# Kernel tuning notes

Measured on AMD Instinct MI355X. Metric: run time of the kernel, lower is better.

The kernel has to match this reference:

```python
import jax, jax.numpy as jnp
import numpy as np

DIM = 1024          # BIGNET_DIM
LORA = 32
GROUP = 128
N_LIN = 18          # 6 blocks * 3 QLoRALinear
N_LN = 5
EPS = 1e-5


def setup_inputs() -> dict:
    key = jax.random.key(0)
    ks = jax.random.split(key, 8)
    tokens = 16384
    x = jax.random.normal(ks[0], (tokens, DIM), dtype=jnp.float32)
    # int4 codes in [0,16), per-(out,group) scale (block-abs-max norm)
    q = jax.random.randint(ks[1], (N_LIN, DIM, DIM), 0, 16, dtype=jnp.int32)
    norm = jax.random.uniform(ks[2], (N_LIN, DIM, DIM // GROUP), dtype=jnp.float32) * 0.1 + 0.01
    bias = jax.random.normal(ks[3], (N_LIN, DIM), dtype=jnp.float32) * 0.01
    # lora_a: kaiming-uniform * 0.01; lora_b: zeros in the original init, but we use
    # small random values so the LoRA path (and its gradients) are exercised.
    lora_a = jax.random.normal(ks[4], (N_LIN, LORA, DIM), dtype=jnp.float32) * 0.01
    lora_b = jax.random.normal(ks[5], (N_LIN, DIM, LORA), dtype=jnp.float32) * 0.01
    ln_gamma = jnp.ones((N_LN, DIM), dtype=jnp.float32)
    ln_beta = jnp.zeros((N_LN, DIM), dtype=jnp.float32)
    return {"x": x, "q": q, "norm": norm, "bias": bias,
            "lora_a": lora_a, "lora_b": lora_b,
            "ln_gamma": ln_gamma, "ln_beta": ln_beta}


def _dequant(qi, ni):
    # qi: [O, I] int codes in [0,16); ni: [O, I//GROUP] group scales
    O, I = qi.shape
    w = (qi.astype(jnp.float32) / 15.0 * 2.0 - 1.0).reshape(O, I // GROUP, GROUP)
    return (w * ni[..., None]).reshape(O, I)


def _qlora_linear(h, qi, ni, b, la, lb):
    w = _dequant(qi, ni)                      # [O, I]
    base = h @ w.T + b                        # frozen quantized path
    lora = (h @ la.T) @ lb.T                  # rank-32 adapter
    return base + lora


def _layernorm(h, g, b):
    mu = jnp.mean(h, axis=-1, keepdims=True)
    var = jnp.var(h, axis=-1, keepdims=True)
    return (h - mu) * jax.lax.rsqrt(var + EPS) * g + b


def _forward(x, q, norm, bias, lora_a, lora_b, ln_gamma, ln_beta):
    h = x
    for blk in range(6):
        r = h
        for j in range(3):
            i = 3 * blk + j
            r = _qlora_linear(r, q[i], norm[i], bias[i], lora_a[i], lora_b[i])
            if j < 2:
                r = jax.nn.relu(r)
        h = r + h                              # residual
        if blk < 5:
            h = _layernorm(h, ln_gamma[blk], ln_beta[blk])
    return h


def reference(x, q, norm, bias, lora_a, lora_b, ln_gamma, ln_beta):
    return _forward(x, q, norm, bias, lora_a, lora_b, ln_gamma, ln_beta)
```

## Files before the change

### kernel.cpp

```cpp
#include <hip/hip_runtime.h>
#include <stdint.h>


#define TOK   16384
#define DIM   1024
#define NLIN  18
#define EPS   1e-5f

typedef _Float16 f16;
typedef _Float16 f16x8 __attribute__((ext_vector_type(8)));
typedef _Float16 f16x4 __attribute__((ext_vector_type(4)));
typedef float    f32x4 __attribute__((ext_vector_type(4)));

__device__ __forceinline__ void load_lds16(const void* g, void* l) {
  __builtin_amdgcn_global_load_lds(
      (const __attribute__((address_space(1))) void*)g,
      (__attribute__((address_space(3))) void*)l,
      16, 0, 0);
}

__global__ __launch_bounds__(256) void prep_w2(
    const int* __restrict__ q, const float* __restrict__ norm,
    const float* __restrict__ la, const float* __restrict__ lb,
    f16* __restrict__ W)
{
  __shared__ float lbs[128 * 32];
  const int bid   = blockIdx.x;
  const int i     = bid >> 5;
  const int ot    = (bid >> 2) & 7;
  const int ktile = bid & 3;
  const int o0 = ot * 128, k0 = ktile * 256;
  const int tid = threadIdx.x;
  const int kg = tid & 63, og = tid >> 6;
  const int k4 = k0 + kg * 4;

  const float* lbsrc = lb + (size_t)i * DIM * 32 + (size_t)o0 * 32;
  #pragma unroll
  for (int p = 0; p < 4; ++p)
    *(float4*)(lbs + p * 1024 + tid * 4) = *(const float4*)(lbsrc + p * 1024 + tid * 4);

  float4 lar[32];
  const float* lasrc = la + (size_t)i * 32 * DIM + k4;
  #pragma unroll
  for (int r = 0; r < 32; ++r) lar[r] = *(const float4*)(lasrc + r * DIM);
  __syncthreads();

  const float s = 2.f / 15.f;
  for (int oi = 0; oi < 32; ++oi) {
    const int o = o0 + og * 32 + oi;
    const size_t wb = ((size_t)i * DIM + o) * DIM;
    const int4 qv = *(const int4*)(q + wb + k4);
    const float nrm = norm[((size_t)i * DIM + o) * 8 + (k4 >> 7)];
    const float* lbr = lbs + (og * 32 + oi) * 32;
    float ax = 0.f, ay = 0.f, az = 0.f, aw = 0.f;
    #pragma unroll
    for (int r = 0; r < 32; ++r) {
      const float b = lbr[r];
      ax += b * lar[r].x; ay += b * lar[r].y; az += b * lar[r].z; aw += b * lar[r].w;
    }
    f16x4 hv;
    hv[0] = (f16)(((float)qv.x * s - 1.f) * nrm + ax);
    hv[1] = (f16)(((float)qv.y * s - 1.f) * nrm + ay);
    hv[2] = (f16)(((float)qv.z * s - 1.f) * nrm + az);
    hv[3] = (f16)(((float)qv.w * s - 1.f) * nrm + aw);
    *(f16x4*)(W + wb + k4) = hv;
  }
}

__global__ __launch_bounds__(256) void cvt_x(
    const float* __restrict__ x, f16* __restrict__ o)
{
  const size_t idx = ((size_t)blockIdx.x * 256 + threadIdx.x) * 4;
  const float4 v = *(const float4*)(x + idx);
  f16x4 h;
  h[0] = (f16)v.x; h[1] = (f16)v.y; h[2] = (f16)v.z; h[3] = (f16)v.w;
  *(f16x4*)(o + idx) = h;
}

#define BARX()   __builtin_amdgcn_s_barrier()
#define LGKM0()  do { asm volatile("s_waitcnt lgkmcnt(0)" ::: "memory"); \
                      __builtin_amdgcn_sched_barrier(0); } while (0)
#define VMC0()   do { asm volatile("s_waitcnt vmcnt(0)" ::: "memory"); \
                      __builtin_amdgcn_sched_barrier(0); } while (0)

#define RD_AF(so, kk) do { \
  _Pragma("unroll") \
  for (int mi = 0; mi < 8; ++mi) \
    af[mi] = *(const f16x8*)(smem + (so) + arowb[mi] + (ckA ^ ((kk) << 6))); \
} while (0)

#define RD_BF(so, ni0, kk) do { \
  bf[ni0]     = *(const f16x8*)(smem + 65536 + (so) + browb[ni0]     + (ckA ^ ((kk) << 6))); \
  bf[(ni0)+1] = *(const f16x8*)(smem + 65536 + (so) + browb[(ni0)+1] + (ckA ^ ((kk) << 6))); \
} while (0)

#define QUAD(ni0) do { \
  __builtin_amdgcn_s_setprio(1); \
  _Pragma("unroll") \
  for (int mi = 0; mi < 8; ++mi) { \
    acc[mi][ni0]     = __builtin_amdgcn_mfma_f32_16x16x32_f16(af[mi], bf[ni0],     acc[mi][ni0],     0, 0, 0); \
    acc[mi][(ni0)+1] = __builtin_amdgcn_mfma_f32_16x16x32_f16(af[mi], bf[(ni0)+1], acc[mi][(ni0)+1], 0, 0, 0); \
  } \
  __builtin_amdgcn_s_setprio(0); \
} while (0)

#define STAGE_A(kt, dstso) do { \
  _Pragma("unroll") \
  for (int qq = 0; qq < 4; ++qq) \
    load_lds16(gA + (size_t)(kt) * 64 + (size_t)qq * 64 * DIM, \
               smem + (dstso) + qq * 8192 + sdst); \
} while (0)
#define STAGE_B(kt, dstso) do { \
  _Pragma("unroll") \
  for (int qq = 0; qq < 4; ++qq) \
    load_lds16(gB + (size_t)(kt) * 64 + (size_t)qq * 64 * DIM, \
               smem + 65536 + (dstso) + qq * 8192 + sdst); \
} while (0)

template<int EPI>
__global__ __launch_bounds__(512, 2) void gemm3(
    const f16* __restrict__ A, const f16* __restrict__ W,
    const float* __restrict__ bias, const f16* __restrict__ resid,
    void* __restrict__ outp)
{
  __shared__ __align__(16) char smem[131072];

  const int orig = blockIdx.x;
  const int swzb = (orig & 7) * 32 + (orig >> 3);
  const int mt = swzb >> 2, nt = swzb & 3;
  const int t0 = mt * 256, n0 = nt * 256;

  const int tid  = threadIdx.x;
  const int lane = tid & 63;
  const int wid  = tid >> 6;
  const int wm = wid >> 2, wn = wid & 3;

  const int srow = tid >> 3;
  const int sch  = (tid & 7) ^ (srow & 7);
  const f16* gA = A + (size_t)(t0 + srow) * DIM + sch * 8;
  const f16* gB = W + (size_t)(n0 + srow) * DIM + sch * 8;
  const int sdst = tid * 16;

  const int ckA = (((lane >> 4) ^ (lane & 7)) << 4);
  int arowb[8], browb[4];
  #pragma unroll
  for (int mi = 0; mi < 8; ++mi)
    arowb[mi] = (wm * 128 + mi * 16 + (lane & 15)) * 128;
  #pragma unroll
  for (int ni = 0; ni < 4; ++ni)
    browb[ni] = (wn * 64 + ni * 16 + (lane & 15)) * 128;

  f32x4 acc[8][4] = {};
  f16x8 af[8], bf[4];

  STAGE_A(0, 0);
  STAGE_B(0, 0);
  VMC0();
  BARX();

  for (int t = 0; t < 16; ++t) {
    const int so = (t & 1) << 15;
    const int od = ((t + 1) & 1) << 15;
    const bool st = (t < 15);
    RD_AF(so, 0); RD_BF(so, 0, 0);
    if (st) STAGE_A(t + 1, od);
    BARX(); LGKM0(); QUAD(0); BARX();
    RD_BF(so, 2, 0);
    if (st) STAGE_B(t + 1, od);
    BARX(); LGKM0(); QUAD(2); BARX();
    RD_AF(so, 1); RD_BF(so, 0, 1);
    BARX(); LGKM0(); QUAD(0); BARX();
    RD_BF(so, 2, 1);
    VMC0();
    BARX(); LGKM0(); QUAD(2); BARX();
  }

  const int colb = lane & 15;
  const int rowb = (lane >> 4) << 2;
  #pragma unroll
  for (int ni = 0; ni < 4; ++ni) {
    const int col = n0 + wn * 64 + ni * 16 + colb;
    const float bv = bias[col];
    #pragma unroll
    for (int mi = 0; mi < 8; ++mi) {
      const int trow = t0 + wm * 128 + mi * 16 + rowb;
      const f32x4 v = acc[mi][ni];
      #pragma unroll
      for (int r = 0; r < 4; ++r) {
        const size_t idx = (size_t)(trow + r) * DIM + col;
        float val = v[r] + bv;
        if constexpr (EPI == 0) {
          val = fmaxf(val, 0.f);
          ((f16*)outp)[idx] = (f16)val;
        } else if constexpr (EPI == 1) {
          val += (float)resid[idx];
          ((f16*)outp)[idx] = (f16)val;
        } else {
          val += (float)resid[idx];
          ((float*)outp)[idx] = val;
        }
      }
    }
  }
}

__global__ __launch_bounds__(256) void ln_k(
    const f16* __restrict__ in, f16* __restrict__ out,
    const float* __restrict__ g, const float* __restrict__ b)
{
  __shared__ float red[8];
  const int row = blockIdx.x;
  const int tid = threadIdx.x;
  const int c = tid * 4;
  const f16x4 v4 = *(const f16x4*)(in + (size_t)row * DIM + c);
  const float v0 = v4[0], v1 = v4[1], v2 = v4[2], v3 = v4[3];
  float s  = v0 + v1 + v2 + v3;
  float s2 = v0 * v0 + v1 * v1 + v2 * v2 + v3 * v3;
  #pragma unroll
  for (int off = 32; off; off >>= 1) {
    s  += __shfl_xor(s,  off);
    s2 += __shfl_xor(s2, off);
  }
  if ((tid & 63) == 0) { red[(tid >> 6) * 2] = s; red[(tid >> 6) * 2 + 1] = s2; }
  __syncthreads();
  s  = red[0] + red[2] + red[4] + red[6];
  s2 = red[1] + red[3] + red[5] + red[7];
  const float mu  = s * (1.f / DIM);
  const float var = fmaxf(s2 * (1.f / DIM) - mu * mu, 0.f);
  const float rs  = rsqrtf(var + EPS);
  const float4 gv = *(const float4*)(g + c);
  const float4 bv = *(const float4*)(b + c);
  f16x4 o4;
  o4[0] = (f16)((v0 - mu) * rs * gv.x + bv.x);
  o4[1] = (f16)((v1 - mu) * rs * gv.y + bv.y);
  o4[2] = (f16)((v2 - mu) * rs * gv.z + bv.z);
  o4[3] = (f16)((v3 - mu) * rs * gv.w + bv.w);
  *(f16x4*)(out + (size_t)row * DIM + c) = o4;
}

extern "C" void kernel_launch(void* const* d_in, const int* in_sizes, int n_in,
                              void* d_out, int out_size, void* d_ws, size_t ws_size,
                              hipStream_t stream)
{
  (void)in_sizes; (void)n_in; (void)out_size; (void)ws_size;
  const float* x     = (const float*)d_in[0];
  const int*   q     = (const int*)d_in[1];
  const float* norm  = (const float*)d_in[2];
  const float* bias  = (const float*)d_in[3];
  const float* la    = (const float*)d_in[4];
  const float* lb    = (const float*)d_in[5];
  const float* lg    = (const float*)d_in[6];
  const float* lbeta = (const float*)d_in[7];

  char* ws = (char*)d_ws;
  f16* W    = (f16*)ws;
  f16* buf1 = (f16*)(ws + (size_t)NLIN * DIM * DIM * 2);
  f16* buf2 = buf1 + (size_t)TOK * DIM;
  f16* buf0 = (f16*)d_out;
  f16* bufs[3] = {buf0, buf1, buf2};

  prep_w2<<<NLIN * 32, 256, 0, stream>>>(q, norm, la, lb, W);
  cvt_x<<<TOK * DIM / 1024, 256, 0, stream>>>(x, buf0);

  int h = 0;
  for (int blk = 0; blk < 6; ++blk) {
    const int a = (h == 0) ? 1 : 0;
    const int p = 3 - h - a;
    const int i0 = blk * 3;
    const size_t wsz = (size_t)DIM * DIM;
    gemm3<0><<<256, 512, 0, stream>>>(bufs[h], W + (i0 + 0) * wsz,
                                      bias + (i0 + 0) * DIM, nullptr, bufs[a]);
    gemm3<0><<<256, 512, 0, stream>>>(bufs[a], W + (i0 + 1) * wsz,
                                      bias + (i0 + 1) * DIM, nullptr, bufs[p]);
    if (blk < 5) {
      gemm3<1><<<256, 512, 0, stream>>>(bufs[p], W + (i0 + 2) * wsz,
                                        bias + (i0 + 2) * DIM, bufs[h], bufs[a]);
      ln_k<<<TOK, 256, 0, stream>>>(bufs[a], bufs[a], lg + blk * DIM, lbeta + blk * DIM);
      h = a;
    } else {
      gemm3<2><<<256, 512, 0, stream>>>(bufs[p], W + (i0 + 2) * wsz,
                                        bias + (i0 + 2) * DIM, bufs[h], d_out);
    }
  }
}
```

Measured before the change: 1.036 ms.

## Restructure GEMM main loop into a register-double-buffered, deeper-prefetch pipeline

Rewrites the GEMM k-loop so LDS fragment reads for the next MFMA quad are issued before the current quad runs, using separate register sets (afX/afY, several B fragment pairs). A-tiles are now prefetched two k-steps ahead and B-tiles one step ahead, with partial vmcnt waits in place of full drains. The LDS layout moves to per-slot A/B halves, and the explicit lgkmcnt waits are removed. The aim is to hide LDS and global latency behind MFMA work, at the cost of more register pressure and a more delicate hazard ordering.

```diff
diff --git a/kernel.cpp b/kernel.cpp
--- a/kernel.cpp
+++ b/kernel.cpp
@@ -77,48 +77,44 @@
   *(f16x4*)(o + idx) = h;
 }
 
-#define BARX()   __builtin_amdgcn_s_barrier()
-#define LGKM0()  do { asm volatile("s_waitcnt lgkmcnt(0)" ::: "memory"); \
-                      __builtin_amdgcn_sched_barrier(0); } while (0)
-#define VMC0()   do { asm volatile("s_waitcnt vmcnt(0)" ::: "memory"); \
-                      __builtin_amdgcn_sched_barrier(0); } while (0)
-
-#define RD_AF(so, kk) do { \
+#define BARX() __builtin_amdgcn_s_barrier()
+
+#define RD_AF(afd, sl, kk) do { \
   _Pragma("unroll") \
   for (int mi = 0; mi < 8; ++mi) \
-    af[mi] = *(const f16x8*)(smem + (so) + arowb[mi] + (ckA ^ ((kk) << 6))); \
-} while (0)
-
-#define RD_BF(so, ni0, kk) do { \
-  bf[ni0]     = *(const f16x8*)(smem + 65536 + (so) + browb[ni0]     + (ckA ^ ((kk) << 6))); \
-  bf[(ni0)+1] = *(const f16x8*)(smem + 65536 + (so) + browb[(ni0)+1] + (ckA ^ ((kk) << 6))); \
-} while (0)
-
-#define QUAD(ni0) do { \
+    afd[mi] = *(const f16x8*)(smem + (sl) + wmbase + arowb[mi] + (ckA ^ ((kk) << 6))); \
+} while (0)
+
+#define RD_BF(b0, b1, sl, np, kk) do { \
+  b0 = *(const f16x8*)(smem + (sl) + 32768 + wnhalf + browb[(np)*2]     + (ckA ^ ((kk) << 6))); \
+  b1 = *(const f16x8*)(smem + (sl) + 32768 + wnhalf + browb[(np)*2 + 1] + (ckA ^ ((kk) << 6))); \
+} while (0)
+
+#define QUAD(afr, b0, b1, nn) do { \
   __builtin_amdgcn_s_setprio(1); \
   _Pragma("unroll") \
   for (int mi = 0; mi < 8; ++mi) { \
-    acc[mi][ni0]     = __builtin_amdgcn_mfma_f32_16x16x32_f16(af[mi], bf[ni0],     acc[mi][ni0],     0, 0, 0); \
-    acc[mi][(ni0)+1] = __builtin_amdgcn_mfma_f32_16x16x32_f16(af[mi], bf[(ni0)+1], acc[mi][(ni0)+1], 0, 0, 0); \
+    acc[mi][nn]     = __builtin_amdgcn_mfma_f32_16x16x32_f16(afr[mi], b0, acc[mi][nn],     0, 0, 0); \
+    acc[mi][(nn)+1] = __builtin_amdgcn_mfma_f32_16x16x32_f16(afr[mi], b1, acc[mi][(nn)+1], 0, 0, 0); \
   } \
   __builtin_amdgcn_s_setprio(0); \
 } while (0)
 
-#define STAGE_A(kt, dstso) do { \
-  _Pragma("unroll") \
-  for (int qq = 0; qq < 4; ++qq) \
-    load_lds16(gA + (size_t)(kt) * 64 + (size_t)qq * 64 * DIM, \
-               smem + (dstso) + qq * 8192 + sdst); \
-} while (0)
-#define STAGE_B(kt, dstso) do { \
-  _Pragma("unroll") \
-  for (int qq = 0; qq < 4; ++qq) \
-    load_lds16(gB + (size_t)(kt) * 64 + (size_t)qq * 64 * DIM, \
-               smem + 65536 + (dstso) + qq * 8192 + sdst); \
+#define STAGE_A(T, h, dslot) do { \
+  load_lds16(gA + (size_t)((T) * 64) + (size_t)((h) * 128) * DIM, \
+             smem + (dslot) + (h) * 16384 + sdst); \
+  load_lds16(gA + (size_t)((T) * 64) + (size_t)((h) * 128 + 64) * DIM, \
+             smem + (dslot) + (h) * 16384 + 8192 + sdst); \
+} while (0)
+#define STAGE_B(T, h, dslot) do { \
+  load_lds16(gB + (size_t)((T) * 64) + (size_t)((h) * 128) * DIM, \
+             smem + (dslot) + 32768 + (h) * 16384 + sdst); \
+  load_lds16(gB + (size_t)((T) * 64) + (size_t)((h) * 128 + 64) * DIM, \
+             smem + (dslot) + 32768 + (h) * 16384 + 8192 + sdst); \
 } while (0)
 
 template<int EPI>
-__global__ __launch_bounds__(512, 2) void gemm3(
+__global__ __launch_bounds__(512, 2) void gemm4(
     const f16* __restrict__ A, const f16* __restrict__ W,
     const float* __restrict__ bias, const f16* __restrict__ resid,
     void* __restrict__ outp)
@@ -141,38 +137,57 @@
   const f16* gB = W + (size_t)(n0 + srow) * DIM + sch * 8;
   const int sdst = tid * 16;
 
-  const int ckA = (((lane >> 4) ^ (lane & 7)) << 4);
+  const int ckA    = (((lane >> 4) ^ (lane & 7)) << 4);
+  const int wmbase = wm * 16384;
+  const int wnhalf = (wn >> 1) * 16384;
   int arowb[8], browb[4];
   #pragma unroll
   for (int mi = 0; mi < 8; ++mi)
-    arowb[mi] = (wm * 128 + mi * 16 + (lane & 15)) * 128;
+    arowb[mi] = (mi * 16 + (lane & 15)) * 128;
   #pragma unroll
   for (int ni = 0; ni < 4; ++ni)
-    browb[ni] = (wn * 64 + ni * 16 + (lane & 15)) * 128;
+    browb[ni] = ((wn & 1) * 64 + ni * 16 + (lane & 15)) * 128;
 
   f32x4 acc[8][4] = {};
-  f16x8 af[8], bf[4];
-
-  STAGE_A(0, 0);
-  STAGE_B(0, 0);
-  VMC0();
+  f16x8 afX[8], afY[8];
+  f16x8 bfP0, bfP1, bfQ0, bfQ1, bfP20, bfP21, bfQ20, bfQ21;
+
+  STAGE_A(0, 0, 0); STAGE_A(0, 1, 0);
+  STAGE_B(0, 0, 0); STAGE_B(0, 1, 0);
+  STAGE_A(1, 0, 65536); STAGE_A(1, 1, 65536);
+  asm volatile("s_waitcnt vmcnt(4)" ::: "memory");
   BARX();
+  RD_AF(afX, 0, 0);
+  RD_BF(bfP0, bfP1, 0, 0, 0);
 
   for (int t = 0; t < 16; ++t) {
-    const int so = (t & 1) << 15;
-    const int od = ((t + 1) & 1) << 15;
-    const bool st = (t < 15);
-    RD_AF(so, 0); RD_BF(so, 0, 0);
-    if (st) STAGE_A(t + 1, od);
-    BARX(); LGKM0(); QUAD(0); BARX();
-    RD_BF(so, 2, 0);
-    if (st) STAGE_B(t + 1, od);
-    BARX(); LGKM0(); QUAD(2); BARX();
-    RD_AF(so, 1); RD_BF(so, 0, 1);
-    BARX(); LGKM0(); QUAD(0); BARX();
-    RD_BF(so, 2, 1);
-    VMC0();
-    BARX(); LGKM0(); QUAD(2); BARX();
+    const int sl = (t & 1) << 16;
+    const int ns = sl ^ 65536;
+    RD_BF(bfQ0, bfQ1, sl, 1, 0);
+    if (t < 15) STAGE_B(t + 1, 0, ns);
+    BARX();
+    QUAD(afX, bfP0, bfP1, 0);
+    RD_AF(afY, sl, 1);
+    RD_BF(bfP20, bfP21, sl, 0, 1);
+    if (t < 15) STAGE_B(t + 1, 1, ns);
+    BARX();
+    QUAD(afX, bfQ0, bfQ1, 2);
+    RD_BF(bfQ20, bfQ21, sl, 1, 1);
+    if (t < 14) STAGE_A(t + 2, 0, sl);
+    BARX();
+    QUAD(afY, bfP20, bfP21, 0);
+    if (t < 14) {
+      STAGE_A(t + 2, 1, sl);
+      asm volatile("s_waitcnt vmcnt(2)" ::: "memory");
+    } else {
+      asm volatile("s_waitcnt vmcnt(0)" ::: "memory");
+    }
+    BARX();
+    if (t < 15) {
+      RD_AF(afX, ns, 0);
+      RD_BF(bfP0, bfP1, ns, 0, 0);
+    }
+    QUAD(afY, bfQ20, bfQ21, 2);
   }
 
   const int colb = lane & 15;
@@ -268,17 +283,17 @@
     const int p = 3 - h - a;
     const int i0 = blk * 3;
     const size_t wsz = (size_t)DIM * DIM;
-    gemm3<0><<<256, 512, 0, stream>>>(bufs[h], W + (i0 + 0) * wsz,
+    gemm4<0><<<256, 512, 0, stream>>>(bufs[h], W + (i0 + 0) * wsz,
                                       bias + (i0 + 0) * DIM, nullptr, bufs[a]);
-    gemm3<0><<<256, 512, 0, stream>>>(bufs[a], W + (i0 + 1) * wsz,
+    gemm4<0><<<256, 512, 0, stream>>>(bufs[a], W + (i0 + 1) * wsz,
                                       bias + (i0 + 1) * DIM, nullptr, bufs[p]);
     if (blk < 5) {
-      gemm3<1><<<256, 512, 0, stream>>>(bufs[p], W + (i0 + 2) * wsz,
+      gemm4<1><<<256, 512, 0, stream>>>(bufs[p], W + (i0 + 2) * wsz,
                                         bias + (i0 + 2) * DIM, bufs[h], bufs[a]);
       ln_k<<<TOK, 256, 0, stream>>>(bufs[a], bufs[a], lg + blk * DIM, lbeta + blk * DIM);
       h = a;
     } else {
-      gemm3<2><<<256, 512, 0, stream>>>(bufs[p], W + (i0 + 2) * wsz,
+      gemm4<2><<<256, 512, 0, stream>>>(bufs[p], W + (i0 + 2) * wsz,
                                         bias + (i0 + 2) * DIM, bufs[h], d_out);
     }
   }
```

New measurement: 981.6 us. -5.2%, faster.
